# Optimization experiments

Measured on AMD Instinct MI355X. Metric: run time of the kernel, lower is better.

## Reference

```python
import jax, jax.numpy as jnp
import numpy as np

N, G, H = 262144, 512, 16
EPS = 1e-5

Q_MAT = jnp.array([[0.0, 0.0, 1.0], [1.0, 0.0, 0.0], [0.0, 1.0, 0.0]], dtype=jnp.float32)
Q_TENSOR = jnp.kron(Q_MAT, Q_MAT)  # 9x9


def setup_inputs() -> dict:
    key = jax.random.key(0)
    ks = jax.random.split(key, 10)
    # sorted node->graph ids, every graph guaranteed non-empty
    gid = jnp.sort(jnp.concatenate([
        jnp.arange(G, dtype=jnp.int32),
        jax.random.randint(ks[0], (N - G,), 0, G, dtype=jnp.int32)]))
    return {
        'x00': jax.random.normal(ks[1], (N, 4 * H), jnp.float32),
        'x10': jax.random.normal(ks[2], (N, H, 3), jnp.float32),
        'x01': jax.random.normal(ks[3], (N, H, 3), jnp.float32),
        'x11': jax.random.normal(ks[4], (N, H, 9), jnp.float32),
        'pos': jax.random.normal(ks[5], (N, 6), jnp.float32),
        'graph_ids': gid,
        'num_graphs': G,
        'bn_gamma': jnp.ones((4 * H,), jnp.float32),
        'bn_beta': jnp.zeros((4 * H,), jnp.float32),
        'lin_w': jax.random.normal(ks[6], (3, 4 * H), jnp.float32) * 0.1,
        'lin_b': jnp.zeros((3,), jnp.float32),
        'w10': jax.random.normal(ks[7], (1, H), jnp.float32) * 0.3,
        'w01': jax.random.normal(ks[8], (1, H), jnp.float32) * 0.3,
        'w11': jax.random.normal(ks[9], (1, H), jnp.float32) * 0.3,
    }


def _graph_norm(x, seg, num_seg, gamma, beta):
    # per-graph mean/var normalization over nodes ('gn')
    cnt = jax.ops.segment_sum(jnp.ones((x.shape[0],), x.dtype), seg, num_segments=num_seg)
    cnt = jnp.maximum(cnt, 1.0)[:, None]
    mean = jax.ops.segment_sum(x, seg, num_segments=num_seg) / cnt
    var = jax.ops.segment_sum(x * x, seg, num_segments=num_seg) / cnt - mean * mean
    xn = (x - mean[seg]) * jax.lax.rsqrt(var[seg] + EPS)
    return xn * gamma + beta


def _segment_softmax(logits, seg, num_seg):
    m = jax.ops.segment_max(logits, seg, num_segments=num_seg)
    e = jnp.exp(logits - m[seg])
    s = jax.ops.segment_sum(e, seg, num_segments=num_seg)
    return e / s[seg]


def _project_r(r_vector):
    # SVD projection to nearest rotation (sign-corrected)
    norm = jnp.clip(jnp.linalg.norm(r_vector, axis=1, keepdims=True), 1e-5, None)
    r_vector = r_vector / jax.lax.stop_gradient(norm)  # norm is detached in torch
    # einops 'b (d c) -> b c d' with c=3
    r_ = jnp.transpose(r_vector.reshape(-1, 3, 3), (0, 2, 1))
    U, S, Vh = jnp.linalg.svd(r_, full_matrices=False)
    rot_pos = U @ Vh
    Vh_neg = Vh.at[:, 2, :].multiply(-1.0)
    rot_neg = U @ Vh_neg
    det = jnp.linalg.det(rot_pos)
    return jnp.where(det[:, None, None] > 0, rot_pos, rot_neg)


def reference(x00, x10, x01, x11, pos, graph_ids, num_graphs,
              bn_gamma, bn_beta, lin_w, lin_b, w10, w01, w11):
    seg = graph_ids
    Gn = num_graphs
    # BN('gn') + Linear -> 3 per-node logits
    xn = _graph_norm(x00, seg, Gn, bn_gamma, bn_beta)
    logits = xn @ lin_w.T + lin_b                       # [N,3]
    W = _segment_softmax(logits, seg, Gn)                # per-graph softmax over nodes
    w0, w1, w2 = W[:, 0:1], W[:, 1:2], W[:, 2:3]
    # weighted per-graph sums (dgl.sum_nodes)
    ab = jnp.concatenate([x10, x01], axis=-1)            # [N,H,6]
    mean_ab = jax.ops.segment_sum(ab * w1[:, :, None], seg, num_segments=Gn)   # [G,H,6]
    r_sum = jax.ops.segment_sum(x11 * w0[:, :, None], seg, num_segments=Gn)    # [G,H,9]
    m1m2 = jax.ops.segment_sum(pos * w2, seg, num_segments=Gn)                 # [G,6]
    m1, m2 = m1m2[:, 0:3], m1m2[:, 3:]
    # GLinear head: channel-mixing H -> 1 per degree type (no bias)
    out10 = jnp.einsum('oc,gcd->god', w10, mean_ab[:, :, :3])[:, 0, :]  # [G,3]
    out01 = jnp.einsum('oc,gcd->god', w01, mean_ab[:, :, 3:6])[:, 0, :]
    out11 = jnp.einsum('oc,gcd->god', w11, r_sum)[:, 0, :]              # [G,9]
    # permutation back to input frame
    r_vector = jnp.einsum('ij,gj->gi', Q_TENSOR, out11)
    trans_b = jnp.einsum('ij,gj->gi', Q_MAT, out01)
    trans_a = jnp.einsum('ij,gj->gi', Q_MAT, out10)
    rot_mat = _project_r(r_vector)
    t = m2 + trans_b - (rot_mat @ m1[..., None])[..., 0] - (rot_mat @ trans_a[..., None])[..., 0]
    return rot_mat, t, r_vector
```

## Files before the change

kernel.cpp:

```cpp
#include <hip/hip_runtime.h>
#include <cstdint>
#include <cstddef>

#define GG 512
#define NF 64
#define EPSF 1e-5f

__device__ __forceinline__ void atomAddF(float* p, float v) {
    unsafeAtomicAdd(p, v);
}

__device__ __forceinline__ void gl_lds16(const float* g, float* l) {
    __builtin_amdgcn_global_load_lds(
        (const __attribute__((address_space(1))) void*)g,
        (__attribute__((address_space(3))) void*)l,
        16, 0, 0);
}

__global__ __launch_bounds__(256) void k_stats(const float* __restrict__ x00, const int* __restrict__ gid,
                        float* __restrict__ gsum, float* __restrict__ gsq,
                        float* __restrict__ gcnt, int N)
{
    int w = (blockIdx.x * blockDim.x + threadIdx.x) >> 6;
    int lane = threadIdx.x & 63;
    long base = (long)w * 64;
    int gf = gid[base];
    int gl = gid[base + 63];
    if (gf == gl) {
        const float4* p = reinterpret_cast<const float4*>(x00 + base * NF) + lane;
        float s0=0,s1=0,s2=0,s3=0,q0=0,q1=0,q2=0,q3=0;
        #pragma unroll
        for (int k = 0; k < 16; ++k) {
            float4 v = p[k * 64];
            s0+=v.x; s1+=v.y; s2+=v.z; s3+=v.w;
            q0=fmaf(v.x,v.x,q0); q1=fmaf(v.y,v.y,q1); q2=fmaf(v.z,v.z,q2); q3=fmaf(v.w,v.w,q3);
        }
        #pragma unroll
        for (int m = 16; m < 64; m <<= 1) {
            s0+=__shfl_xor(s0,m); s1+=__shfl_xor(s1,m); s2+=__shfl_xor(s2,m); s3+=__shfl_xor(s3,m);
            q0+=__shfl_xor(q0,m); q1+=__shfl_xor(q1,m); q2+=__shfl_xor(q2,m); q3+=__shfl_xor(q3,m);
        }
        if (lane < 16) {
            float* ds = gsum + gf * NF + lane * 4;
            float* dq = gsq  + gf * NF + lane * 4;
            atomAddF(ds+0,s0); atomAddF(ds+1,s1); atomAddF(ds+2,s2); atomAddF(ds+3,s3);
            atomAddF(dq+0,q0); atomAddF(dq+1,q1); atomAddF(dq+2,q2); atomAddF(dq+3,q3);
        }
        if (lane == 0) atomAddF(&gcnt[gf], 64.0f);
    } else {
        int myg = gid[base + lane];
        int cur = gf;
        float s = 0.f, q = 0.f, cnt = 0.f;
        for (int k = 0; k < 64; ++k) {
            int g = __shfl(myg, k);
            if (g != cur) {
                atomAddF(&gsum[cur * NF + lane], s);
                atomAddF(&gsq [cur * NF + lane], q);
                if (lane == 0) atomAddF(&gcnt[cur], cnt);
                s = q = cnt = 0.f; cur = g;
            }
            float v = x00[(base + k) * NF + lane];
            s += v; q = fmaf(v, v, q); cnt += 1.f;
        }
        atomAddF(&gsum[cur * NF + lane], s);
        atomAddF(&gsq [cur * NF + lane], q);
        if (lane == 0) atomAddF(&gcnt[cur], cnt);
    }
}

__global__ void k_prep(const float* __restrict__ gsum, const float* __restrict__ gsq,
                       const float* __restrict__ gcnt,
                       const float* __restrict__ gamma, const float* __restrict__ beta,
                       const float* __restrict__ lin_w, const float* __restrict__ lin_b,
                       float* __restrict__ Aeff, float* __restrict__ Beff)
{
    int g = blockIdx.x;
    int c = threadIdx.x;
    float cnt = fmaxf(gcnt[g], 1.f);
    float mean = gsum[g * NF + c] / cnt;
    float var  = gsq [g * NF + c] / cnt - mean * mean;
    float rs = rsqrtf(var + EPSF);
    float ga = gamma[c], be = beta[c];
    #pragma unroll
    for (int j = 0; j < 3; ++j) {
        float wv = lin_w[j * NF + c];
        Aeff[((long)g * 3 + j) * NF + c] = rs * ga * wv;
        float term = (be - mean * rs * ga) * wv;
        #pragma unroll
        for (int m = 32; m; m >>= 1) term += __shfl_xor(term, m);
        if (c == 0) Beff[g * 3 + j] = term + lin_b[j];
    }
}

__global__ __launch_bounds__(128) void k_logits(const float* __restrict__ x00, const int* __restrict__ gid,
                         const float* __restrict__ pos,
                         const float* __restrict__ Aeff, const float* __restrict__ Beff,
                         float* __restrict__ ebp, float* __restrict__ accum, int N)
{
    __shared__ float T2[2][64 * 68];
    int wid = threadIdx.x >> 6;
    int lane = threadIdx.x & 63;
    long chunk = (long)blockIdx.x * 2 + wid;
    long base = chunk * 64;
    float* T = T2[wid];

    const float* src = x00 + base * NF;
    #pragma unroll
    for (int k = 0; k < 16; ++k) {
        int fl = k * 256 + lane * 4;
        float4 v = *reinterpret_cast<const float4*>(src + fl);
        int n = fl >> 6, c = fl & 63;
        *reinterpret_cast<float4*>(&T[n * 68 + c]) = v;
    }
    __syncthreads();

    int gf = gid[base], gl = gid[base + 63];
    float l0, l1, l2;
    int g_l;
    if (gf == gl) {
        g_l = gf;
        const float* ap = Aeff + (size_t)gf * 192;
        float a0a=0,a0b=0,a1a=0,a1b=0,a2a=0,a2b=0;
        #pragma unroll
        for (int t = 0; t < 16; ++t) {
            float4 xv = *reinterpret_cast<const float4*>(&T[lane * 68 + 4 * t]);
            float4 w0 = *reinterpret_cast<const float4*>(ap + 4 * t);
            float4 w1 = *reinterpret_cast<const float4*>(ap + 64 + 4 * t);
            float4 w2 = *reinterpret_cast<const float4*>(ap + 128 + 4 * t);
            a0a = fmaf(xv.x,w0.x,fmaf(xv.y,w0.y,a0a)); a0b = fmaf(xv.z,w0.z,fmaf(xv.w,w0.w,a0b));
            a1a = fmaf(xv.x,w1.x,fmaf(xv.y,w1.y,a1a)); a1b = fmaf(xv.z,w1.z,fmaf(xv.w,w1.w,a1b));
            a2a = fmaf(xv.x,w2.x,fmaf(xv.y,w2.y,a2a)); a2b = fmaf(xv.z,w2.z,fmaf(xv.w,w2.w,a2b));
        }
        l0 = a0a + a0b + Beff[gf*3+0];
        l1 = a1a + a1b + Beff[gf*3+1];
        l2 = a2a + a2b + Beff[gf*3+2];
    } else {
        g_l = gid[base + lane];
        const float* ap = Aeff + (size_t)g_l * 192;
        float a0=0,a1=0,a2=0;
        #pragma unroll
        for (int t = 0; t < 16; ++t) {
            float4 xv = *reinterpret_cast<const float4*>(&T[lane * 68 + 4 * t]);
            float4 w0 = *reinterpret_cast<const float4*>(ap + 4 * t);
            float4 w1 = *reinterpret_cast<const float4*>(ap + 64 + 4 * t);
            float4 w2 = *reinterpret_cast<const float4*>(ap + 128 + 4 * t);
            a0 = fmaf(xv.x,w0.x,fmaf(xv.y,w0.y,fmaf(xv.z,w0.z,fmaf(xv.w,w0.w,a0))));
            a1 = fmaf(xv.x,w1.x,fmaf(xv.y,w1.y,fmaf(xv.z,w1.z,fmaf(xv.w,w1.w,a1))));
            a2 = fmaf(xv.x,w2.x,fmaf(xv.y,w2.y,fmaf(xv.z,w2.z,fmaf(xv.w,w2.w,a2))));
        }
        l0 = a0 + Beff[g_l*3+0];
        l1 = a1 + Beff[g_l*3+1];
        l2 = a2 + Beff[g_l*3+2];
    }
    float e0 = expf(l0), e1 = expf(l1), e2 = expf(l2);
    long node = base + lane;
    ebp[node]            = e0;
    ebp[(long)N + node]  = e1;

    const float* pp = pos + node * 6;
    float2 v01 = *reinterpret_cast<const float2*>(pp);
    float2 v23 = *reinterpret_cast<const float2*>(pp + 2);
    float2 v45 = *reinterpret_cast<const float2*>(pp + 4);
    float p0 = v01.x*e2, p1 = v01.y*e2, p2 = v23.x*e2, p3 = v23.y*e2, p4 = v45.x*e2, p5 = v45.y*e2;
    if (gf == gl) {
        #pragma unroll
        for (int m = 1; m < 64; m <<= 1) {
            e0+=__shfl_xor(e0,m); e1+=__shfl_xor(e1,m); e2+=__shfl_xor(e2,m);
            p0+=__shfl_xor(p0,m); p1+=__shfl_xor(p1,m); p2+=__shfl_xor(p2,m);
            p3+=__shfl_xor(p3,m); p4+=__shfl_xor(p4,m); p5+=__shfl_xor(p5,m);
        }
        if (lane == 0) {
            float* dst = accum + (long)gf * 32;
            atomAddF(dst+16,p0); atomAddF(dst+17,p1); atomAddF(dst+18,p2);
            atomAddF(dst+19,p3); atomAddF(dst+20,p4); atomAddF(dst+21,p5);
            atomAddF(dst+22,e0); atomAddF(dst+23,e1); atomAddF(dst+24,e2);
        }
    } else {
        float* dst = accum + (long)g_l * 32;
        atomAddF(dst+16,p0); atomAddF(dst+17,p1); atomAddF(dst+18,p2);
        atomAddF(dst+19,p3); atomAddF(dst+20,p4); atomAddF(dst+21,p5);
        atomAddF(dst+22,e0); atomAddF(dst+23,e1); atomAddF(dst+24,e2);
    }
}

__global__ __launch_bounds__(256) void k_wsum(const float* __restrict__ x10,
        const float* __restrict__ x01, const float* __restrict__ x11,
        const float* __restrict__ ebp, const int* __restrict__ gid,
        const float* __restrict__ w10, const float* __restrict__ w01,
        const float* __restrict__ w11, float* __restrict__ accum, int N)
{
    __shared__ float SMEM[4752];
    const int tid = threadIdx.x;
    const int wid = tid >> 6;
    const int lane = tid & 63;
    const int T = 16;

    if ((blockIdx.x & 1) == 0) {
        const long blkBase = (long)(blockIdx.x >> 1) * 256;
        float* LD0 = SMEM;
        float* LD1 = SMEM + 2304;
        float* F   = SMEM + 4608;

        float w[16];
        #pragma unroll
        for (int c = 0; c < 16; ++c) w[c] = w11[c];

        const bool act = tid < 144;
        const int n1 = (act ? tid : 0) / 9;
        const int d1 = (act ? tid : 0) - 9 * ((act ? tid : 0) / 9);

        float acc1 = 0.f;
        int cur = gid[blkBase];
        bool dirty = false;

        auto flush = [&]() {
            if (dirty) {
                if (act) F[tid] = acc1;
                __syncthreads();
                if (tid < 9) {
                    float s = 0.f;
                    #pragma unroll
                    for (int n = 0; n < 16; ++n) s += F[n * 9 + tid];
                    atomAddF(accum + (long)cur * 32 + 6 + tid, s);
                }
                __syncthreads();
                acc1 = 0.f;
                dirty = false;
            }
        };

        auto issueT = [&](int t, int b) {
            const float* src = x11 + (blkBase + (long)t * 16) * 144;
            float* dst = b ? LD1 : LD0;
            gl_lds16(src + (wid)     * 256 + lane * 4, dst + (wid)     * 256);
            gl_lds16(src + (wid + 4) * 256 + lane * 4, dst + (wid + 4) * 256);
            if (wid == 0)
                gl_lds16(src + 8 * 256 + lane * 4, dst + 8 * 256);
        };

        issueT(0, 0);
        __syncthreads();

        for (int t = 0; t < T; ++t) {
            if (t + 1 < T) issueT(t + 1, (t + 1) & 1);
            const float* B = (t & 1) ? LD1 : LD0;
            long tb = blkBase + (long)t * 16;
            int gf = gid[tb], gl = gid[tb + 15];
            float y1 = 0.f, ev = 0.f;
            if (act) {
                ev = ebp[tb + n1];
                #pragma unroll
                for (int c = 0; c < 16; ++c) y1 = fmaf(w[c], B[n1 * 144 + c * 9 + d1], y1);
            }
            if (gf == gl) {
                if (gf != cur) { flush(); cur = gf; }
                if (act) acc1 = fmaf(ev, y1, acc1);
                dirty = true;
            } else {
                flush();
                if (act) atomAddF(accum + (long)gid[tb + n1] * 32 + 6 + d1, ev * y1);
                cur = gl;
            }
            __syncthreads();
        }
        flush();
    } else {
        const long blkBase = (long)(blockIdx.x >> 1) * 256;
        float* LD0 = SMEM;
        float* LD1 = SMEM + 1536;
        float* F   = SMEM + 3072;

        const bool act = tid < 96;
        const int arr = (tid < 48) ? 0 : 1;
        const int rem = (act ? (tid - 48 * arr) : 0);
        const int nn = rem / 3;
        const int dd = rem - 3 * (rem / 3);

        float wsel[16];
        #pragma unroll
        for (int c = 0; c < 16; ++c) wsel[c] = arr ? w01[c] : w10[c];

        float acc = 0.f;
        int cur = gid[blkBase];
        bool dirty = false;

        auto flush = [&]() {
            if (dirty) {
                if (act) F[tid] = acc;
                __syncthreads();
                if (tid < 6) {
                    int a = tid / 3, d = tid - 3 * a;
                    float s = 0.f;
                    #pragma unroll
                    for (int n = 0; n < 16; ++n) s += F[a * 48 + n * 3 + d];
                    atomAddF(accum + (long)cur * 32 + a * 3 + d, s);
                }
                __syncthreads();
                acc = 0.f;
                dirty = false;
            }
        };

        auto issueT = [&](int t, int b) {
            long tb16 = (blkBase + (long)t * 16) * 48;
            float* dst = b ? LD1 : LD0;
            {
                int s = wid;
                const float* g = (s < 3) ? (x10 + tb16 + s * 256)
                                         : (x01 + tb16 + (s - 3) * 256);
                float* l = (s < 3) ? (dst + s * 256) : (dst + 768 + (s - 3) * 256);
                gl_lds16(g + lane * 4, l);
            }
            if (wid < 2) {
                int s = wid + 4;
                const float* g = x01 + tb16 + (s - 3) * 256;
                float* l = dst + 768 + (s - 3) * 256;
                gl_lds16(g + lane * 4, l);
            }
        };

        issueT(0, 0);
        __syncthreads();

        for (int t = 0; t < T; ++t) {
            if (t + 1 < T) issueT(t + 1, (t + 1) & 1);
            const float* Bx = ((t & 1) ? LD1 : LD0) + arr * 768;
            long tb = blkBase + (long)t * 16;
            int gf = gid[tb], gl = gid[tb + 15];
            float y = 0.f, ev = 0.f;
            if (act) {
                ev = ebp[(long)N + tb + nn];
                #pragma unroll
                for (int c = 0; c < 16; ++c) y = fmaf(wsel[c], Bx[nn * 48 + c * 3 + dd], y);
            }
            if (gf == gl) {
                if (gf != cur) { flush(); cur = gf; }
                if (act) acc = fmaf(ev, y, acc);
                dirty = true;
            } else {
                flush();
                if (act) atomAddF(accum + (long)gid[tb + nn] * 32 + arr * 3 + dd, ev * y);
                cur = gl;
            }
            __syncthreads();
        }
        flush();
    }
}

#define JROT(p, q) do { \
    float apq_ = S[p][q]; \
    if (fabsf(apq_) > 1e-20f) { \
        float app_ = S[p][p], aqq_ = S[q][q]; \
        float tau_ = (aqq_ - app_) / (2.0f * apq_); \
        float tt_ = copysignf(1.0f, tau_) / (fabsf(tau_) + sqrtf(1.0f + tau_ * tau_)); \
        float cc_ = 1.0f / sqrtf(1.0f + tt_ * tt_); \
        float ssn_ = tt_ * cc_; \
        _Pragma("unroll") for (int kk = 0; kk < 3; ++kk) { \
            float skp = S[kk][p], skq = S[kk][q]; \
            S[kk][p] = cc_ * skp - ssn_ * skq; S[kk][q] = ssn_ * skp + cc_ * skq; } \
        _Pragma("unroll") for (int kk = 0; kk < 3; ++kk) { \
            float spk = S[p][kk], sqk = S[q][kk]; \
            S[p][kk] = cc_ * spk - ssn_ * sqk; S[q][kk] = ssn_ * spk + cc_ * sqk; } \
        _Pragma("unroll") for (int kk = 0; kk < 3; ++kk) { \
            float vkp = V[kk][p], vkq = V[kk][q]; \
            V[kk][p] = cc_ * vkp - ssn_ * vkq; V[kk][q] = ssn_ * vkp + cc_ * vkq; } \
    } \
} while (0)

__global__ void k_final(const float* __restrict__ accum, float* __restrict__ out)
{
    int g = blockIdx.x * blockDim.x + threadIdx.x;
    if (g >= GG) return;
    const float* A_ = accum + (long)g * 32;
    float i0 = 1.f / A_[22], i1 = 1.f / A_[23], i2 = 1.f / A_[24];

    float o10[3], o01[3], o11[9];
    #pragma unroll
    for (int d = 0; d < 3; ++d) { o10[d] = A_[d] * i1; o01[d] = A_[3 + d] * i1; }
    #pragma unroll
    for (int d = 0; d < 9; ++d) o11[d] = A_[6 + d] * i0;

    float m1v[3], m2v[3];
    #pragma unroll
    for (int d = 0; d < 3; ++d) { m1v[d] = A_[16 + d] * i2; m2v[d] = A_[19 + d] * i2; }

    int sig[3]; sig[0] = 2; sig[1] = 0; sig[2] = 1;
    float rv[9];
    #pragma unroll
    for (int a = 0; a < 3; ++a)
        #pragma unroll
        for (int b = 0; b < 3; ++b)
            rv[a * 3 + b] = o11[sig[a] * 3 + sig[b]];
    float ta[3], tb[3];
    #pragma unroll
    for (int a = 0; a < 3; ++a) { ta[a] = o10[sig[a]]; tb[a] = o01[sig[a]]; }

    float nn = 0.f;
    #pragma unroll
    for (int k = 0; k < 9; ++k) nn += rv[k] * rv[k];
    float invn = 1.f / fmaxf(sqrtf(nn), 1e-5f);
    float M[3][3];
    #pragma unroll
    for (int a = 0; a < 3; ++a)
        #pragma unroll
        for (int b = 0; b < 3; ++b)
            M[a][b] = rv[b * 3 + a] * invn;

    float S[3][3], V[3][3];
    #pragma unroll
    for (int a = 0; a < 3; ++a)
        #pragma unroll
        for (int b = 0; b < 3; ++b) {
            float acc = 0.f;
            #pragma unroll
            for (int k = 0; k < 3; ++k) acc += M[k][a] * M[k][b];
            S[a][b] = acc;
            V[a][b] = (a == b) ? 1.f : 0.f;
        }
    for (int sw = 0; sw < 12; ++sw) { JROT(0, 1); JROT(0, 2); JROT(1, 2); }

    float l0 = S[0][0], l1 = S[1][1], l2 = S[2][2];
    float e0x = V[0][0], e0y = V[1][0], e0z = V[2][0];
    float e1x = V[0][1], e1y = V[1][1], e1z = V[2][1];
    float e2x = V[0][2], e2y = V[1][2], e2z = V[2][2];
    float tfl;
    if (l0 < l1) { tfl=l0;l0=l1;l1=tfl; tfl=e0x;e0x=e1x;e1x=tfl; tfl=e0y;e0y=e1y;e1y=tfl; tfl=e0z;e0z=e1z;e1z=tfl; }
    if (l0 < l2) { tfl=l0;l0=l2;l2=tfl; tfl=e0x;e0x=e2x;e2x=tfl; tfl=e0y;e0y=e2y;e2y=tfl; tfl=e0z;e0z=e2z;e2z=tfl; }
    if (l1 < l2) { tfl=l1;l1=l2;l2=tfl; tfl=e1x;e1x=e2x;e2x=tfl; tfl=e1y;e1y=e2y;e2y=tfl; tfl=e1z;e1z=e2z;e2z=tfl; }

    float c2x = e0y * e1z - e0z * e1y;
    float c2y = e0z * e1x - e0x * e1z;
    float c2z = e0x * e1y - e0y * e1x;
    float cn = rsqrtf(fmaxf(c2x * c2x + c2y * c2y + c2z * c2z, 1e-30f));
    c2x *= cn; c2y *= cn; c2z *= cn;

    float u0x = M[0][0] * e0x + M[0][1] * e0y + M[0][2] * e0z;
    float u0y = M[1][0] * e0x + M[1][1] * e0y + M[1][2] * e0z;
    float u0z = M[2][0] * e0x + M[2][1] * e0y + M[2][2] * e0z;
    float un = rsqrtf(fmaxf(u0x * u0x + u0y * u0y + u0z * u0z, 1e-30f));
    u0x *= un; u0y *= un; u0z *= un;
    float u1x = M[0][0] * e1x + M[0][1] * e1y + M[0][2] * e1z;
    float u1y = M[1][0] * e1x + M[1][1] * e1y + M[1][2] * e1z;
    float u1z = M[2][0] * e1x + M[2][1] * e1y + M[2][2] * e1z;
    float dp = u0x * u1x + u0y * u1y + u0z * u1z;
    u1x -= dp * u0x; u1y -= dp * u0y; u1z -= dp * u0z;
    un = rsqrtf(fmaxf(u1x * u1x + u1y * u1y + u1z * u1z, 1e-30f));
    u1x *= un; u1y *= un; u1z *= un;
    float u2x = u0y * u1z - u0z * u1y;
    float u2y = u0z * u1x - u0x * u1z;
    float u2z = u0x * u1y - u0y * u1x;

    float R[3][3];
    R[0][0] = u0x * e0x + u1x * e1x + u2x * c2x;
    R[0][1] = u0x * e0y + u1x * e1y + u2x * c2y;
    R[0][2] = u0x * e0z + u1x * e1z + u2x * c2z;
    R[1][0] = u0y * e0x + u1y * e1x + u2y * c2x;
    R[1][1] = u0y * e0y + u1y * e1y + u2y * c2y;
    R[1][2] = u0y * e0z + u1y * e1z + u2y * c2z;
    R[2][0] = u0z * e0x + u1z * e1x + u2z * c2x;
    R[2][1] = u0z * e0y + u1z * e1y + u2z * c2y;
    R[2][2] = u0z * e0z + u1z * e1z + u2z * c2z;

    float tv[3];
    #pragma unroll
    for (int a = 0; a < 3; ++a) {
        float acc = m2v[a] + tb[a];
        #pragma unroll
        for (int b = 0; b < 3; ++b) acc -= R[a][b] * (m1v[b] + ta[b]);
        tv[a] = acc;
    }

    #pragma unroll
    for (int k = 0; k < 9; ++k) out[(long)g * 9 + k] = R[k / 3][k % 3];
    #pragma unroll
    for (int a = 0; a < 3; ++a) out[(long)GG * 9 + (long)g * 3 + a] = tv[a];
    #pragma unroll
    for (int k = 0; k < 9; ++k) out[(long)GG * 12 + (long)g * 9 + k] = rv[k];
}

extern "C" void kernel_launch(void* const* d_in, const int* in_sizes, int n_in,
                              void* d_out, int out_size, void* d_ws, size_t ws_size,
                              hipStream_t stream)
{
    const float* x00   = (const float*)d_in[0];
    const float* x10   = (const float*)d_in[1];
    const float* x01   = (const float*)d_in[2];
    const float* x11   = (const float*)d_in[3];
    const float* pos   = (const float*)d_in[4];
    const int*   gid   = (const int*)d_in[5];
    const float* gamma = (const float*)d_in[7];
    const float* beta  = (const float*)d_in[8];
    const float* lin_w = (const float*)d_in[9];
    const float* lin_b = (const float*)d_in[10];
    const float* w10   = (const float*)d_in[11];
    const float* w01   = (const float*)d_in[12];
    const float* w11   = (const float*)d_in[13];
    float* out = (float*)d_out;

    const int N = in_sizes[0] / NF;

    float* ws = (float*)d_ws;
    float* gsum  = ws;
    float* gsq   = gsum + GG * 64;
    float* gcnt  = gsq + GG * 64;
    float* accum = gcnt + GG;
    float* Aeff  = accum + GG * 32;
    float* Beff  = Aeff + GG * 192;
    float* ebp   = Beff + GG * 3;

    size_t zeroBytes = (size_t)(GG * 64 * 2 + GG + GG * 32) * sizeof(float);
    hipMemsetAsync(d_ws, 0, zeroBytes, stream);

    int blocksA = (N / 64) / 4;
    int blocksL = (N / 64) / 2;
    int blocksD = 2 * (N / 256);

    k_stats <<<blocksA, 256, 0, stream>>>(x00, gid, gsum, gsq, gcnt, N);
    k_prep  <<<GG, 64, 0, stream>>>(gsum, gsq, gcnt, gamma, beta, lin_w, lin_b, Aeff, Beff);
    k_logits<<<blocksL, 128, 0, stream>>>(x00, gid, pos, Aeff, Beff, ebp, accum, N);
    k_wsum  <<<blocksD, 256, 0, stream>>>(x10, x01, x11, ebp, gid, w10, w01, w11, accum, N);
    k_final <<<(GG + 63) / 64, 64, 0, stream>>>(accum, out);
}
```

Baseline: 169.2 us.

## Triple-buffer k_wsum LDS loads with vmcnt waits and stage ebp via LDS

Replaces the double-buffered global-to-LDS pipeline in k_wsum with a three-stage ring buffer. Each iteration now syncs with per-wave s_waitcnt vmcnt plus a raw s_barrier instead of a trailing __syncthreads. The softmax weights (ebp) are also loaded asynchronously into LDS alongside the tiles rather than read from global memory in the compute loop. The goal is to keep two tiles of loads in flight and cut barrier stalls, at the cost of more shared memory and fragile hand-tuned waitcnt counts that must match each wave's issued loads.

```diff
diff --git a/kernel.cpp b/kernel.cpp
--- a/kernel.cpp
+++ b/kernel.cpp
@@ -13,8 +13,21 @@
 __device__ __forceinline__ void gl_lds16(const float* g, float* l) {
     __builtin_amdgcn_global_load_lds(
         (const __attribute__((address_space(1))) void*)g,
-        (__attribute__((address_space(3))) void*)l,
-        16, 0, 0);
+        (__attribute__((address_space(3))) void*)l, 16, 0, 0);
+}
+__device__ __forceinline__ void gl_lds4(const float* g, float* l) {
+    __builtin_amdgcn_global_load_lds(
+        (const __attribute__((address_space(1))) void*)g,
+        (__attribute__((address_space(3))) void*)l, 4, 0, 0);
+}
+
+__device__ __forceinline__ void waitv(int n) {
+    switch (n) {
+        case 0: asm volatile("s_waitcnt vmcnt(0)" ::: "memory"); break;
+        case 1: asm volatile("s_waitcnt vmcnt(1)" ::: "memory"); break;
+        case 2: asm volatile("s_waitcnt vmcnt(2)" ::: "memory"); break;
+        default: asm volatile("s_waitcnt vmcnt(3)" ::: "memory"); break;
+    }
 }
 
 __global__ __launch_bounds__(256) void k_stats(const float* __restrict__ x00, const int* __restrict__ gid,
@@ -189,7 +202,7 @@
         const float* __restrict__ w10, const float* __restrict__ w01,
         const float* __restrict__ w11, float* __restrict__ accum, int N)
 {
-    __shared__ float SMEM[4752];
+    __shared__ float SMEM[7104];
     const int tid = threadIdx.x;
     const int wid = tid >> 6;
     const int lane = tid & 63;
@@ -197,9 +210,7 @@
 
     if ((blockIdx.x & 1) == 0) {
         const long blkBase = (long)(blockIdx.x >> 1) * 256;
-        float* LD0 = SMEM;
-        float* LD1 = SMEM + 2304;
-        float* F   = SMEM + 4608;
+        float* F = SMEM + 6960;
 
         float w[16];
         #pragma unroll
@@ -208,6 +219,7 @@
         const bool act = tid < 144;
         const int n1 = (act ? tid : 0) / 9;
         const int d1 = (act ? tid : 0) - 9 * ((act ? tid : 0) / 9);
+        const int Sw = (wid == 0 || wid == 3) ? 3 : 2;
 
         float acc1 = 0.f;
         int cur = gid[blkBase];
@@ -229,26 +241,41 @@
             }
         };
 
-        auto issueT = [&](int t, int b) {
-            const float* src = x11 + (blkBase + (long)t * 16) * 144;
-            float* dst = b ? LD1 : LD0;
-            gl_lds16(src + (wid)     * 256 + lane * 4, dst + (wid)     * 256);
-            gl_lds16(src + (wid + 4) * 256 + lane * 4, dst + (wid + 4) * 256);
-            if (wid == 0)
+        auto issueT = [&](int t) {
+            const long tb = blkBase + (long)t * 16;
+            const float* src = x11 + tb * 144;
+            float* dst = SMEM + (t % 3) * 2320;
+            if (wid == 0) {
+                gl_lds16(src + 0 * 256 + lane * 4, dst + 0 * 256);
+                gl_lds16(src + 1 * 256 + lane * 4, dst + 1 * 256);
                 gl_lds16(src + 8 * 256 + lane * 4, dst + 8 * 256);
+            } else if (wid == 1) {
+                gl_lds16(src + 2 * 256 + lane * 4, dst + 2 * 256);
+                gl_lds16(src + 3 * 256 + lane * 4, dst + 3 * 256);
+            } else if (wid == 2) {
+                gl_lds16(src + 4 * 256 + lane * 4, dst + 4 * 256);
+                gl_lds16(src + 5 * 256 + lane * 4, dst + 5 * 256);
+            } else {
+                gl_lds16(src + 6 * 256 + lane * 4, dst + 6 * 256);
+                gl_lds16(src + 7 * 256 + lane * 4, dst + 7 * 256);
+                if (lane < 16) gl_lds4(ebp + tb + lane, dst + 2304);
+            }
         };
 
-        issueT(0, 0);
-        __syncthreads();
+        issueT(0);
+        issueT(1);
 
         for (int t = 0; t < T; ++t) {
-            if (t + 1 < T) issueT(t + 1, (t + 1) & 1);
-            const float* B = (t & 1) ? LD1 : LD0;
+            waitv(t == T - 1 ? 0 : Sw);
+            __builtin_amdgcn_s_barrier();
+            __builtin_amdgcn_sched_barrier(0);
+            if (t + 2 < T) issueT(t + 2);
+            const float* B = SMEM + (t % 3) * 2320;
             long tb = blkBase + (long)t * 16;
             int gf = gid[tb], gl = gid[tb + 15];
             float y1 = 0.f, ev = 0.f;
             if (act) {
-                ev = ebp[tb + n1];
+                ev = B[2304 + n1];
                 #pragma unroll
                 for (int c = 0; c < 16; ++c) y1 = fmaf(w[c], B[n1 * 144 + c * 9 + d1], y1);
             }
@@ -261,20 +288,18 @@
                 if (act) atomAddF(accum + (long)gid[tb + n1] * 32 + 6 + d1, ev * y1);
                 cur = gl;
             }
-            __syncthreads();
         }
         flush();
     } else {
         const long blkBase = (long)(blockIdx.x >> 1) * 256;
-        float* LD0 = SMEM;
-        float* LD1 = SMEM + 1536;
-        float* F   = SMEM + 3072;
+        float* F = SMEM + 4656;
 
         const bool act = tid < 96;
         const int arr = (tid < 48) ? 0 : 1;
         const int rem = (act ? (tid - 48 * arr) : 0);
         const int nn = rem / 3;
         const int dd = rem - 3 * (rem / 3);
+        const int Sw = (wid == 3) ? 1 : 2;
 
         float wsel[16];
         #pragma unroll
@@ -301,35 +326,39 @@
             }
         };
 
-        auto issueT = [&](int t, int b) {
-            long tb16 = (blkBase + (long)t * 16) * 48;
-            float* dst = b ? LD1 : LD0;
-            {
-                int s = wid;
-                const float* g = (s < 3) ? (x10 + tb16 + s * 256)
-                                         : (x01 + tb16 + (s - 3) * 256);
-                float* l = (s < 3) ? (dst + s * 256) : (dst + 768 + (s - 3) * 256);
-                gl_lds16(g + lane * 4, l);
-            }
-            if (wid < 2) {
-                int s = wid + 4;
-                const float* g = x01 + tb16 + (s - 3) * 256;
-                float* l = dst + 768 + (s - 3) * 256;
-                gl_lds16(g + lane * 4, l);
+        auto issueT = [&](int t) {
+            const long tb = blkBase + (long)t * 16;
+            const long tb48 = tb * 48;
+            float* dst = SMEM + (t % 3) * 1552;
+            if (wid == 0) {
+                gl_lds16(x10 + tb48 + 0 * 256 + lane * 4, dst + 0 * 256);
+                gl_lds16(x10 + tb48 + 1 * 256 + lane * 4, dst + 1 * 256);
+            } else if (wid == 1) {
+                gl_lds16(x10 + tb48 + 2 * 256 + lane * 4, dst + 2 * 256);
+                gl_lds16(x01 + tb48 + 0 * 256 + lane * 4, dst + 768);
+            } else if (wid == 2) {
+                gl_lds16(x01 + tb48 + 1 * 256 + lane * 4, dst + 768 + 256);
+                gl_lds16(x01 + tb48 + 2 * 256 + lane * 4, dst + 768 + 512);
+            } else {
+                if (lane < 16) gl_lds4(ebp + (long)N + tb + lane, dst + 1536);
             }
         };
 
-        issueT(0, 0);
-        __syncthreads();
+        issueT(0);
+        issueT(1);
 
         for (int t = 0; t < T; ++t) {
-            if (t + 1 < T) issueT(t + 1, (t + 1) & 1);
-            const float* Bx = ((t & 1) ? LD1 : LD0) + arr * 768;
+            waitv(t == T - 1 ? 0 : Sw);
+            __builtin_amdgcn_s_barrier();
+            __builtin_amdgcn_sched_barrier(0);
+            if (t + 2 < T) issueT(t + 2);
+            const float* D = SMEM + (t % 3) * 1552;
+            const float* Bx = D + arr * 768;
             long tb = blkBase + (long)t * 16;
             int gf = gid[tb], gl = gid[tb + 15];
             float y = 0.f, ev = 0.f;
             if (act) {
-                ev = ebp[(long)N + tb + nn];
+                ev = D[1536 + nn];
                 #pragma unroll
                 for (int c = 0; c < 16; ++c) y = fmaf(wsel[c], Bx[nn * 48 + c * 3 + dd], y);
             }
@@ -342,7 +371,6 @@
                 if (act) atomAddF(accum + (long)gid[tb + nn] * 32 + arr * 3 + dd, ev * y);
                 cur = gl;
             }
-            __syncthreads();
         }
         flush();
     }
```

Result: no change. 168.4 us, median of 2 (-0.5%).
